# Performance work log

Hardware: AMD Instinct MI355X
Metric: run time of the kernel (lower is better)

The kernel has to match this reference:

```python
import jax, jax.numpy as jnp
import numpy as np

B, N = 256, 512
DIM_GRAPH = 256
DIM_DESC = 256
RANK = 64


def setup_inputs() -> dict:
    key = jax.random.key(0)
    ks = jax.random.split(key, 6)
    tokns_k = jax.random.normal(ks[0], (B, DIM_DESC), dtype=jnp.float32)
    H_pad = jax.random.normal(ks[1], (B, N, DIM_GRAPH), dtype=jnp.float32)
    mask = jax.random.randint(ks[2], (B, N), 0, 2).astype(bool)
    mask = mask.at[:, 0].set(True)  # ensure at least one valid node per graph
    # Linear weights, torch convention: y = x @ W.T
    Wq = jax.random.normal(ks[3], (RANK, DIM_DESC), dtype=jnp.float32) / np.sqrt(DIM_DESC)
    Wk = jax.random.normal(ks[4], (RANK, DIM_GRAPH), dtype=jnp.float32) / np.sqrt(DIM_GRAPH)
    Wv = jax.random.normal(ks[5], (DIM_DESC, DIM_GRAPH), dtype=jnp.float32) / np.sqrt(DIM_GRAPH)
    log_scale = jnp.zeros((1,), dtype=jnp.float32)
    return {"tokns_k": tokns_k, "H_pad": H_pad, "mask": mask,
            "Wq": Wq, "Wk": Wk, "Wv": Wv, "log_scale": log_scale}


def reference(tokns_k, H_pad, mask, Wq, Wk, Wv, log_scale):
    q = tokns_k @ Wq.T                                  # [B, r]
    k = jnp.einsum('bnd,rd->bnr', H_pad, Wk)            # [B, N, r]
    scale = jnp.maximum(jnp.exp(log_scale), 0.1)        # clamp(min=0.1)
    scores = jnp.einsum('br,bnr->bn', q, k) / scale     # [B, N]
    neg_inf = jnp.float32(-jnp.inf)
    scores = jnp.where(mask, scores, neg_inf)
    alpha = jax.nn.softmax(scores, axis=-1)             # [B, N]
    v = jnp.einsum('bnd,ed->bne', H_pad, Wv)            # [B, N, dim_desc]
    ctx_k = jnp.einsum('bn,bne->be', alpha, v)          # [B, dim_desc]
    return (alpha, ctx_k)
```

## Files before the change

### kernel.cpp

```cpp
#include <hip/hip_runtime.h>

constexpr int Bc = 256;
constexpr int Nc = 512;
constexpr int Dc = 256;
constexpr int Rc = 64;
constexpr int SPLIT = 8;
constexpr int ROWS = Nc / SPLIT;

typedef float f4 __attribute__((ext_vector_type(4)));

constexpr size_t WS_P = 0;
constexpr size_t WS_L = WS_P + (size_t)Bc * Dc;
constexpr size_t WS_H = WS_L + (size_t)Bc * SPLIT;
constexpr size_t WS_FLOATS = WS_H + (size_t)Bc * SPLIT * Dc;

__global__ __launch_bounds__(256) void k0_precompute_p(
    const float* __restrict__ tokns_k, const float* __restrict__ Wq,
    const float* __restrict__ Wk, float* __restrict__ ws)
{
    const int b = blockIdx.x;
    const int t = threadIdx.x;
    const int wave = t >> 6, lane = t & 63, g = lane >> 4, l16 = lane & 15;

    __shared__ float q_s[Rc];

    #pragma unroll
    for (int step = 0; step < 4; ++step) {
        const int r = wave * 16 + step * 4 + g;
        float acc = 0.0f;
        #pragma unroll
        for (int j = 0; j < 4; ++j) {
            const float4 tk = *(const float4*)(tokns_k + b * Dc + l16 * 4 + j * 64);
            const float4 wq = *(const float4*)(Wq + r * Dc + l16 * 4 + j * 64);
            acc += tk.x * wq.x + tk.y * wq.y + tk.z * wq.z + tk.w * wq.w;
        }
        #pragma unroll
        for (int off = 1; off < 16; off <<= 1) acc += __shfl_xor(acc, off);
        if (l16 == 0) q_s[r] = acc;
    }
    __syncthreads();

    float acc = 0.0f;
    #pragma unroll 8
    for (int r = 0; r < Rc; ++r) acc += q_s[r] * Wk[r * Dc + t];
    ws[WS_P + (size_t)b * Dc + t] = acc;
}

__global__ __launch_bounds__(256) void k1_stream(
    const float* __restrict__ H_pad, const int* __restrict__ mask,
    const float* __restrict__ log_scale, float* __restrict__ ws,
    float* __restrict__ out)
{
    const int s = blockIdx.x;
    const int b = blockIdx.y;
    const int t = threadIdx.x;
    const int wave = t >> 6, lane = t & 63, g = lane >> 4, l16 = lane & 15;
    const int n0 = s * ROWS;

    __shared__ __align__(16) float hm[16][Dc];
    __shared__ float l_s[16];
    __shared__ float scores_s[ROWS];
    __shared__ int   mask_s[ROWS];

    if (t < ROWS) mask_s[t] = mask[b * Nc + n0 + t];

    const float inv_scale = 1.0f / fmaxf(__expf(log_scale[0]), 0.1f);

    const float* __restrict__ pb = ws + WS_P + (size_t)b * Dc;
    float4 p4[4];
    #pragma unroll
    for (int j = 0; j < 4; ++j) p4[j] = *(const float4*)(pb + l16 * 4 + j * 64);
    __syncthreads();

    const float* __restrict__ Hb = H_pad + ((size_t)b * Nc + n0) * Dc;
    float  l_acc = 0.0f;
    float4 h4[4];
    #pragma unroll
    for (int j = 0; j < 4; ++j) h4[j] = make_float4(0.f, 0.f, 0.f, 0.f);

    #pragma unroll
    for (int step = 0; step < 4; ++step) {
        const int nr = step * 16 + wave * 4 + g;
        if (mask_s[nr] != 0) {
            const float* __restrict__ row = Hb + nr * Dc + l16 * 4;
            f4 x[4];
            #pragma unroll
            for (int j = 0; j < 4; ++j)
                x[j] = __builtin_nontemporal_load((const f4*)(row + j * 64));

            float s0 = x[0][0] * p4[0].x + x[0][1] * p4[0].y + x[0][2] * p4[0].z + x[0][3] * p4[0].w;
            float s1 = x[1][0] * p4[1].x + x[1][1] * p4[1].y + x[1][2] * p4[1].z + x[1][3] * p4[1].w;
            float s2 = x[2][0] * p4[2].x + x[2][1] * p4[2].y + x[2][2] * p4[2].z + x[2][3] * p4[2].w;
            float s3 = x[3][0] * p4[3].x + x[3][1] * p4[3].y + x[3][2] * p4[3].z + x[3][3] * p4[3].w;
            float sc = (s0 + s1) + (s2 + s3);
            #pragma unroll
            for (int off = 1; off < 16; off <<= 1) sc += __shfl_xor(sc, off);
            sc *= inv_scale;
            if (l16 == 0) scores_s[nr] = sc;

            const float pn = __expf(sc);
            l_acc += pn;
            #pragma unroll
            for (int j = 0; j < 4; ++j) {
                h4[j].x = fmaf(pn, x[j][0], h4[j].x);
                h4[j].y = fmaf(pn, x[j][1], h4[j].y);
                h4[j].z = fmaf(pn, x[j][2], h4[j].z);
                h4[j].w = fmaf(pn, x[j][3], h4[j].w);
            }
        } else {
            if (l16 == 0) scores_s[nr] = -1e30f;
        }
    }

    const int team = wave * 4 + g;
    #pragma unroll
    for (int j = 0; j < 4; ++j) *(float4*)(&hm[team][l16 * 4 + j * 64]) = h4[j];
    if (l16 == 0) l_s[team] = l_acc;
    __syncthreads();

    if (t < ROWS) out[b * Nc + n0 + t] = scores_s[t];
    float hsum = 0.0f;
    #pragma unroll
    for (int p = 0; p < 16; ++p) hsum += hm[p][t];
    ws[WS_H + ((size_t)b * SPLIT + s) * Dc + t] = hsum;
    if (t == 0) {
        float L = 0.0f;
        #pragma unroll
        for (int p = 0; p < 16; ++p) L += l_s[p];
        ws[WS_L + (size_t)b * SPLIT + s] = L;
    }
}

__global__ __launch_bounds__(256) void k2_merge(
    const float* __restrict__ Wv, const float* __restrict__ ws,
    float* __restrict__ out)
{
    const int b = blockIdx.x;
    const int t = threadIdx.x;
    const int wave = t >> 6, lane = t & 63, g = lane >> 4, l16 = lane & 15;

    __shared__ __align__(16) float hbar[Dc];

    float L = 0.0f;
    #pragma unroll
    for (int s = 0; s < SPLIT; ++s) L += ws[WS_L + (size_t)b * SPLIT + s];
    const float invL = 1.0f / L;

    float hacc = 0.0f;
    #pragma unroll
    for (int s = 0; s < SPLIT; ++s) hacc += ws[WS_H + ((size_t)b * SPLIT + s) * Dc + t];
    hbar[t] = hacc * invL;

    #pragma unroll
    for (int i = 0; i < Nc / 256; ++i) {
        const int idx = b * Nc + i * 256 + t;
        out[idx] = __expf(out[idx]) * invL;
    }
    __syncthreads();

    float4 hb4[4];
    #pragma unroll
    for (int j = 0; j < 4; ++j) hb4[j] = *(const float4*)(hbar + l16 * 4 + j * 64);
    float* __restrict__ ctx_out = out + (size_t)Bc * Nc + b * Dc;
    #pragma unroll
    for (int step = 0; step < 16; ++step) {
        const int e = step * 16 + wave * 4 + g;
        float acc = 0.0f;
        #pragma unroll
        for (int j = 0; j < 4; ++j) {
            const float4 wv = *(const float4*)(Wv + e * Dc + l16 * 4 + j * 64);
            acc += wv.x * hb4[j].x + wv.y * hb4[j].y + wv.z * hb4[j].z + wv.w * hb4[j].w;
        }
        #pragma unroll
        for (int off = 1; off < 16; off <<= 1) acc += __shfl_xor(acc, off);
        if (l16 == 0) ctx_out[e] = acc;
    }
}

constexpr int FNT = 512;
constexpr int FNW = FNT / 64;
constexpr int FNPW = Nc / FNW;

__global__ __launch_bounds__(FNT) void fba_fallback(
    const float* __restrict__ tokns_k, const float* __restrict__ H_pad,
    const int* __restrict__ mask, const float* __restrict__ Wq,
    const float* __restrict__ Wk, const float* __restrict__ Wv,
    const float* __restrict__ log_scale, float* __restrict__ out)
{
    const int b = blockIdx.x, t = threadIdx.x;
    const int wave = t >> 6, lane = t & 63;

    __shared__ __align__(16) float q_s[Rc];
    __shared__ __align__(16) float p_s[Dc];
    __shared__ __align__(16) float scores_s[Nc];
    __shared__ __align__(16) float hmerge[FNW][Dc];
    __shared__ float l_s[FNW];
    __shared__ __align__(16) float hbar[Dc];
    __shared__ int mask_s[Nc];

    const float inv_scale = 1.0f / fmaxf(__expf(log_scale[0]), 0.1f);

    const float4 tok4 = *(const float4*)(tokns_k + b * Dc + lane * 4);
    #pragma unroll
    for (int i = 0; i < Rc / FNW; ++i) {
        const int r = wave * (Rc / FNW) + i;
        const float4 w4 = *(const float4*)(Wq + r * Dc + lane * 4);
        float s = w4.x * tok4.x + w4.y * tok4.y + w4.z * tok4.z + w4.w * tok4.w;
        #pragma unroll
        for (int off = 32; off >= 1; off >>= 1) s += __shfl_xor(s, off);
        if (lane == 0) q_s[r] = s;
    }
    mask_s[t] = mask[b * Nc + t];
    mask_s[t + FNT] = mask[b * Nc + t + FNT];
    __syncthreads();

    if (t < Dc) {
        float acc = 0.0f;
        #pragma unroll 8
        for (int r = 0; r < Rc; ++r) acc += q_s[r] * Wk[r * Dc + t];
        p_s[t] = acc;
    }
    __syncthreads();

    const float4 p4 = *(const float4*)(p_s + lane * 4);
    const float* Hb = H_pad + (size_t)b * Nc * Dc;
    float l_acc = 0.0f;
    float4 h4 = make_float4(0.f, 0.f, 0.f, 0.f);

    for (int i = 0; i < FNPW; ++i) {
        const int n = wave * FNPW + i;
        const float4 x4 = *(const float4*)(Hb + n * Dc + lane * 4);
        float s = x4.x * p4.x + x4.y * p4.y + x4.z * p4.z + x4.w * p4.w;
        #pragma unroll
        for (int off = 32; off >= 1; off >>= 1) s += __shfl_xor(s, off);
        s *= inv_scale;
        if (mask_s[n] == 0) s = -1e30f;
        if (lane == 0) scores_s[n] = s;
        const float pn = __expf(s);
        l_acc += pn;
        h4.x = fmaf(pn, x4.x, h4.x); h4.y = fmaf(pn, x4.y, h4.y);
        h4.z = fmaf(pn, x4.z, h4.z); h4.w = fmaf(pn, x4.w, h4.w);
    }

    if (lane == 0) l_s[wave] = l_acc;
    *(float4*)(&hmerge[wave][lane * 4]) = h4;
    __syncthreads();

    float L = 0.0f;
    #pragma unroll
    for (int w = 0; w < FNW; ++w) L += l_s[w];
    const float invL = 1.0f / L;

    if (t < Dc) {
        float acc = 0.0f;
        #pragma unroll
        for (int w = 0; w < FNW; ++w) acc += hmerge[w][t];
        hbar[t] = acc * invL;
    }
    out[b * Nc + t] = __expf(scores_s[t]) * invL;
    out[b * Nc + t + FNT] = __expf(scores_s[t + FNT]) * invL;
    __syncthreads();

    const float4 hb4 = *(const float4*)(hbar + lane * 4);
    float* ctx_out = out + (size_t)Bc * Nc + b * Dc;
    #pragma unroll
    for (int i = 0; i < Dc / FNW; ++i) {
        const int e = wave * (Dc / FNW) + i;
        const float4 w4 = *(const float4*)(Wv + e * Dc + lane * 4);
        float s = w4.x * hb4.x + w4.y * hb4.y + w4.z * hb4.z + w4.w * hb4.w;
        #pragma unroll
        for (int off = 32; off >= 1; off >>= 1) s += __shfl_xor(s, off);
        if (lane == 0) ctx_out[e] = s;
    }
}

extern "C" void kernel_launch(void* const* d_in, const int* in_sizes, int n_in,
                              void* d_out, int out_size, void* d_ws, size_t ws_size,
                              hipStream_t stream) {
    const float* tokns_k   = (const float*)d_in[0];
    const float* H_pad     = (const float*)d_in[1];
    const int*   mask      = (const int*)d_in[2];
    const float* Wq        = (const float*)d_in[3];
    const float* Wk        = (const float*)d_in[4];
    const float* Wv        = (const float*)d_in[5];
    const float* log_scale = (const float*)d_in[6];
    float* out = (float*)d_out;

    if (ws_size >= WS_FLOATS * sizeof(float)) {
        float* ws = (float*)d_ws;
        k0_precompute_p<<<Bc, 256, 0, stream>>>(tokns_k, Wq, Wk, ws);
        dim3 grid1(SPLIT, Bc);
        k1_stream<<<grid1, 256, 0, stream>>>(H_pad, mask, log_scale, ws, out);
        k2_merge<<<Bc, 256, 0, stream>>>(Wv, ws, out);
    } else {
        fba_fallback<<<Bc, FNT, 0, stream>>>(tokns_k, H_pad, mask, Wq, Wk, Wv,
                                             log_scale, out);
    }
}
```

Before: 205.2 us.

## Halve split count and double-buffer row loads in streaming kernel

Reduces SPLIT from 8 to 4, so each block processes 128 rows (8 steps) instead of 64. The row loop is restructured into a two-buffer software pipeline that issues the next row's loads before processing the current row, with mask bits precomputed into a bitmask. The intent is more memory-level parallelism per thread and fewer partial results to combine, at the cost of half as many blocks (1024) and higher register pressure.

```diff
diff --git a/kernel.cpp b/kernel.cpp
--- a/kernel.cpp
+++ b/kernel.cpp
@@ -4,8 +4,9 @@
 constexpr int Nc = 512;
 constexpr int Dc = 256;
 constexpr int Rc = 64;
-constexpr int SPLIT = 8;
+constexpr int SPLIT = 4;
 constexpr int ROWS = Nc / SPLIT;
+constexpr int NSTEP = ROWS / 16;
 
 typedef float f4 __attribute__((ext_vector_type(4)));
 
@@ -56,6 +57,7 @@
     const int t = threadIdx.x;
     const int wave = t >> 6, lane = t & 63, g = lane >> 4, l16 = lane & 15;
     const int n0 = s * ROWS;
+    const int team = wave * 4 + g;
 
     __shared__ __align__(16) float hm[16][Dc];
     __shared__ float l_s[16];
@@ -72,47 +74,66 @@
     for (int j = 0; j < 4; ++j) p4[j] = *(const float4*)(pb + l16 * 4 + j * 64);
     __syncthreads();
 
+    int actbits = 0;
+    #pragma unroll
+    for (int k = 0; k < NSTEP; ++k)
+        actbits |= (mask_s[k * 16 + team] != 0) ? (1 << k) : 0;
+
     const float* __restrict__ Hb = H_pad + ((size_t)b * Nc + n0) * Dc;
     float  l_acc = 0.0f;
     float4 h4[4];
     #pragma unroll
     for (int j = 0; j < 4; ++j) h4[j] = make_float4(0.f, 0.f, 0.f, 0.f);
 
-    #pragma unroll
-    for (int step = 0; step < 4; ++step) {
-        const int nr = step * 16 + wave * 4 + g;
-        if (mask_s[nr] != 0) {
+    auto LOADROW = [&](f4 (&x)[4], int nr, bool act) {
+        if (act) {
             const float* __restrict__ row = Hb + nr * Dc + l16 * 4;
-            f4 x[4];
             #pragma unroll
             for (int j = 0; j < 4; ++j)
                 x[j] = __builtin_nontemporal_load((const f4*)(row + j * 64));
-
-            float s0 = x[0][0] * p4[0].x + x[0][1] * p4[0].y + x[0][2] * p4[0].z + x[0][3] * p4[0].w;
-            float s1 = x[1][0] * p4[1].x + x[1][1] * p4[1].y + x[1][2] * p4[1].z + x[1][3] * p4[1].w;
-            float s2 = x[2][0] * p4[2].x + x[2][1] * p4[2].y + x[2][2] * p4[2].z + x[2][3] * p4[2].w;
-            float s3 = x[3][0] * p4[3].x + x[3][1] * p4[3].y + x[3][2] * p4[3].z + x[3][3] * p4[3].w;
-            float sc = (s0 + s1) + (s2 + s3);
-            #pragma unroll
-            for (int off = 1; off < 16; off <<= 1) sc += __shfl_xor(sc, off);
-            sc *= inv_scale;
-            if (l16 == 0) scores_s[nr] = sc;
-
-            const float pn = __expf(sc);
-            l_acc += pn;
-            #pragma unroll
-            for (int j = 0; j < 4; ++j) {
-                h4[j].x = fmaf(pn, x[j][0], h4[j].x);
-                h4[j].y = fmaf(pn, x[j][1], h4[j].y);
-                h4[j].z = fmaf(pn, x[j][2], h4[j].z);
-                h4[j].w = fmaf(pn, x[j][3], h4[j].w);
-            }
-        } else {
+        }
+    };
+    auto PROCROW = [&](const f4 (&x)[4], int nr, bool act) {
+        if (!act) {
             if (l16 == 0) scores_s[nr] = -1e30f;
-        }
-    }
-
-    const int team = wave * 4 + g;
+            return;
+        }
+        float s0 = x[0][0] * p4[0].x + x[0][1] * p4[0].y + x[0][2] * p4[0].z + x[0][3] * p4[0].w;
+        float s1 = x[1][0] * p4[1].x + x[1][1] * p4[1].y + x[1][2] * p4[1].z + x[1][3] * p4[1].w;
+        float s2 = x[2][0] * p4[2].x + x[2][1] * p4[2].y + x[2][2] * p4[2].z + x[2][3] * p4[2].w;
+        float s3 = x[3][0] * p4[3].x + x[3][1] * p4[3].y + x[3][2] * p4[3].z + x[3][3] * p4[3].w;
+        float sc = (s0 + s1) + (s2 + s3);
+        #pragma unroll
+        for (int off = 1; off < 16; off <<= 1) sc += __shfl_xor(sc, off);
+        sc *= inv_scale;
+        if (l16 == 0) scores_s[nr] = sc;
+
+        const float pn = __expf(sc);
+        l_acc += pn;
+        #pragma unroll
+        for (int j = 0; j < 4; ++j) {
+            h4[j].x = fmaf(pn, x[j][0], h4[j].x);
+            h4[j].y = fmaf(pn, x[j][1], h4[j].y);
+            h4[j].z = fmaf(pn, x[j][2], h4[j].z);
+            h4[j].w = fmaf(pn, x[j][3], h4[j].w);
+        }
+    };
+
+    f4 xa[4], xb[4];
+    LOADROW(xa, team, (actbits >> 0) & 1);
+    #pragma unroll
+    for (int it = 0; it < NSTEP / 2; ++it) {
+        const int nrA = it * 32 + team;
+        const int nrB = nrA + 16;
+        const bool actA = (actbits >> (2 * it)) & 1;
+        const bool actB = (actbits >> (2 * it + 1)) & 1;
+        LOADROW(xb, nrB, actB);
+        PROCROW(xa, nrA, actA);
+        if (it + 1 < NSTEP / 2)
+            LOADROW(xa, nrA + 32, (actbits >> (2 * it + 2)) & 1);
+        PROCROW(xb, nrB, actB);
+    }
+
     #pragma unroll
     for (int j = 0; j < 4; ++j) *(float4*)(&hm[team][l16 * 4 + j * 64]) = h4[j];
     if (l16 == 0) l_s[team] = l_acc;
```

After: 202.4 us. About the same (-1.4%).
